# Kernel tuning notes

Hardware: AMD Instinct MI355X
Metric: run time of the kernel (lower is better)

Reference implementation:

```python
import jax, jax.numpy as jnp
import numpy as np

D_MODEL = 768
BOTTLENECK = 64
LN_EPS = 1e-5
SCALE = 1.0


def setup_inputs() -> dict:
    key = jax.random.key(0)
    k_x, k_wd = jax.random.split(key, 2)
    x = jax.random.normal(k_x, (8, 4096, D_MODEL), dtype=jnp.float32)
    # LayerNorm params (torch default init: weight=1, bias=0)
    ln_w = jnp.ones((D_MODEL,), dtype=jnp.float32)
    ln_b = jnp.zeros((D_MODEL,), dtype=jnp.float32)
    # down_proj: kaiming_uniform(a=sqrt(5)) -> bound = 1/sqrt(fan_in)
    bound = 1.0 / np.sqrt(D_MODEL)
    w_down = jax.random.uniform(k_wd, (BOTTLENECK, D_MODEL), dtype=jnp.float32,
                                minval=-bound, maxval=bound)
    b_down = jnp.zeros((BOTTLENECK,), dtype=jnp.float32)
    # up_proj initialized to zeros per the module; use small random values
    # instead so the backward test is non-degenerate? No: stay faithful but
    # zeros would kill gradients through w_down; use a tiny random up matrix
    # (mathematically same op, just different param values).
    k_wu = jax.random.fold_in(key, 7)
    w_up = 0.02 * jax.random.normal(k_wu, (D_MODEL, BOTTLENECK), dtype=jnp.float32)
    b_up = jnp.zeros((D_MODEL,), dtype=jnp.float32)
    return {"x": x, "ln_w": ln_w, "ln_b": ln_b,
            "w_down": w_down, "b_down": b_down,
            "w_up": w_up, "b_up": b_up}


def reference(x, ln_w, ln_b, w_down, b_down, w_up, b_up):
    # adapter_layernorm_option == 'in': LayerNorm first
    mu = jnp.mean(x, axis=-1, keepdims=True)
    var = jnp.mean(jnp.square(x - mu), axis=-1, keepdims=True)
    xn = (x - mu) * jax.lax.rsqrt(var + LN_EPS) * ln_w + ln_b
    # down projection + ReLU (dropout p=0 in eval -> identity)
    down = jax.nn.relu(jnp.einsum('bsd,kd->bsk', xn, w_down) + b_down)
    # up projection, scale, residual add (add_residual=True, residual=x)
    up = (jnp.einsum('bsk,dk->bsd', down, w_up) + b_up) * SCALE
    return up + x
```

## Files before the change

### kernel.cpp

```cpp
#include <hip/hip_runtime.h>

#define D_MODEL 768
#define BN 64
#define LN_EPS 1e-5f

typedef __attribute__((ext_vector_type(8))) short bf16x8;
typedef __attribute__((ext_vector_type(4))) float f32x4;

static __device__ __forceinline__ unsigned short f2bf(float f) {
    unsigned int u = __float_as_uint(f);
    u = (u + 0x7FFFu + ((u >> 16) & 1u)) >> 16;
    return (unsigned short)u;
}
static __device__ __forceinline__ float bf2f(unsigned short u) {
    return __uint_as_float(((unsigned int)u) << 16);
}

__global__ void prep(const float* __restrict__ wd, const float* __restrict__ ln_w,
                     const float* __restrict__ ln_b, const float* __restrict__ b_down,
                     const float* __restrict__ wu,
                     unsigned short* __restrict__ wd2_frag, unsigned short* __restrict__ wu_frag,
                     float* __restrict__ S, float* __restrict__ bd2) {
    const int b = blockIdx.x;
    const int t = threadIdx.x;
    const int c = b;
    const int wv = c >> 4, cl = c & 15;
    float s = 0.f, sb = 0.f;
    #pragma unroll
    for (int i = 0; i < 12; ++i) {
        const int d = t + 64 * i;
        const float w0 = wd[c * D_MODEL + d];
        const float w2 = w0 * ln_w[d];
        s  += w2;
        sb += w0 * ln_b[d];
        const int ks = d >> 5, kg = (d >> 3) & 3, e = d & 7;
        wd2_frag[(((wv * 24 + ks) * 64) + kg * 16 + cl) * 8 + e] = f2bf(w2);
    }
    #pragma unroll
    for (int off = 1; off < 64; off <<= 1) {
        s  += __shfl_xor(s, off);
        sb += __shfl_xor(sb, off);
    }
    if (t == 0) { S[c] = s; bd2[c] = b_down[c] + sb; }
    #pragma unroll
    for (int i = 0; i < 12; ++i) {
        const int n = b * 12 + i;
        const float v = wu[n * BN + t];
        const int jj = n >> 4, nl = n & 15;
        const int h = t >> 5, kg = (t >> 3) & 3, e = t & 7;
        wu_frag[(((jj * 2 + h) * 64) + kg * 16 + nl) * 8 + e] = f2bf(v);
    }
}

__global__ __launch_bounds__(256, 4) void adapter_kernel(
    const float* __restrict__ x,
    const unsigned short* __restrict__ wd2_frag, const float* __restrict__ S,
    const float* __restrict__ bd2,
    const unsigned short* __restrict__ wu_frag, const float* __restrict__ b_up,
    float* __restrict__ out)
{
    __shared__ __align__(16) unsigned short sX[16 * 768];
    __shared__ __align__(16) unsigned short sDown[16][72];
    __shared__ float sMu[16], sRs[16];

    const int tid  = threadIdx.x;
    const int lane = tid & 63;
    const int w    = tid >> 6;
    const int kg   = lane >> 4;
    const int l16  = lane & 15;
    const size_t gt0 = (size_t)blockIdx.x * 16;

    {
        float4 v[12];
        const float* base0 = x + (gt0 + w * 4) * D_MODEL + lane * 4;
        #pragma unroll
        for (int p = 0; p < 4; ++p) {
            #pragma unroll
            for (int sg = 0; sg < 3; ++sg)
                v[p * 3 + sg] = *(const float4*)(base0 + p * D_MODEL + sg * 256);
        }
        #pragma unroll
        for (int p = 0; p < 4; ++p) {
            const int r = w * 4 + p;
            float sum = 0.f, sq = 0.f;
            #pragma unroll
            for (int sg = 0; sg < 3; ++sg) {
                const float4 f = v[p * 3 + sg];
                sum += (f.x + f.y) + (f.z + f.w);
                sq  += (f.x * f.x + f.y * f.y) + (f.z * f.z + f.w * f.w);
            }
            #pragma unroll
            for (int off = 1; off < 64; off <<= 1) {
                sum += __shfl_xor(sum, off);
                sq  += __shfl_xor(sq, off);
            }
            if (lane == 0) {
                const float mu = sum * (1.f / D_MODEL);
                sMu[r] = mu;
                sRs[r] = rsqrtf(sq * (1.f / D_MODEL) - mu * mu + LN_EPS);
            }
            #pragma unroll
            for (int sg = 0; sg < 3; ++sg) {
                const float4 f = v[p * 3 + sg];
                ushort4 o;
                o.x = f2bf(f.x); o.y = f2bf(f.y); o.z = f2bf(f.z); o.w = f2bf(f.w);
                const int bytecol = ((sg * 256 + lane * 4) * 2) ^ ((r & 15) << 4);
                *(ushort4*)((char*)&sX[r * 768] + bytecol) = o;
            }
        }
    }
    __syncthreads();

    {
        const int c = w * 16 + l16;
        const unsigned short* bp = wd2_frag + ((size_t)(w * 24) * 64 + lane) * 8;
        const char* sxrow = (const char*)&sX[l16 * 768];
        f32x4 acc = {0.f, 0.f, 0.f, 0.f};
        #pragma unroll
        for (int ks = 0; ks < 24; ++ks) {
            const bf16x8 a = *(const bf16x8*)(sxrow + ((ks * 64 + kg * 16) ^ (l16 << 4)));
            const bf16x8 b = *(const bf16x8*)(bp + ks * 512);
            acc = __builtin_amdgcn_mfma_f32_16x16x32_bf16(a, b, acc, 0, 0, 0);
        }
        const float Sc = S[c], bd = bd2[c];
        #pragma unroll
        for (int r = 0; r < 4; ++r) {
            const int t = kg * 4 + r;
            const float vv = sRs[t] * (acc[r] - sMu[t] * Sc) + bd;
            sDown[t][c] = f2bf(vv > 0.f ? vv : 0.f);
        }
    }
    __syncthreads();

    {
        const bf16x8 pb0 = *(const bf16x8*)&sDown[l16][kg * 8];
        const bf16x8 pb1 = *(const bf16x8*)&sDown[l16][32 + kg * 8];
        float* orow = out + (gt0 + l16) * D_MODEL;
        const char* sxrow = (const char*)&sX[l16 * 768];
        #pragma unroll 3
        for (int j = 0; j < 12; ++j) {
            const int jj = 4 * j + w;
            const unsigned short* ap = wu_frag + ((size_t)(jj * 2) * 64 + lane) * 8;
            const bf16x8 a0 = *(const bf16x8*)ap;
            const bf16x8 a1 = *(const bf16x8*)(ap + 512);
            f32x4 acc = {0.f, 0.f, 0.f, 0.f};
            acc = __builtin_amdgcn_mfma_f32_16x16x32_bf16(a0, pb0, acc, 0, 0, 0);
            acc = __builtin_amdgcn_mfma_f32_16x16x32_bf16(a1, pb1, acc, 0, 0, 0);
            const int oc = jj * 16 + kg * 4;
            const float4 bu = *(const float4*)(b_up + oc);
            const ushort4 xb = *(const ushort4*)(sxrow + ((oc * 2) ^ (l16 << 4)));
            float4 o;
            o.x = acc[0] + bu.x + bf2f(xb.x);
            o.y = acc[1] + bu.y + bf2f(xb.y);
            o.z = acc[2] + bu.z + bf2f(xb.z);
            o.w = acc[3] + bu.w + bf2f(xb.w);
            *(float4*)(orow + oc) = o;
        }
    }
}

extern "C" void kernel_launch(void* const* d_in, const int* in_sizes, int n_in,
                              void* d_out, int out_size, void* d_ws, size_t ws_size,
                              hipStream_t stream) {
    const float* x      = (const float*)d_in[0];
    const float* ln_w   = (const float*)d_in[1];
    const float* ln_b   = (const float*)d_in[2];
    const float* w_down = (const float*)d_in[3];
    const float* b_down = (const float*)d_in[4];
    const float* w_up   = (const float*)d_in[5];
    const float* b_up   = (const float*)d_in[6];
    float* out = (float*)d_out;

    unsigned short* wd2_frag = (unsigned short*)d_ws;
    unsigned short* wu_frag  = wd2_frag + BN * D_MODEL;
    float* S   = (float*)((char*)d_ws + 2 * BN * D_MODEL * sizeof(unsigned short));
    float* bd2 = S + BN;

    prep<<<BN, 64, 0, stream>>>(w_down, ln_w, ln_b, b_down, w_up, wd2_frag, wu_frag, S, bd2);

    const int tokens = in_sizes[0] / D_MODEL;
    const int grid = tokens / 16;
    adapter_kernel<<<grid, 256, 0, stream>>>(x, wd2_frag, S, bd2, wu_frag, b_up, out);
}
```

Before: 50.51 us.

## Process two token tiles per block, prefetching the second tile during GEMMs

Each block now handles two 16-token tiles, so the grid is halved. The second tile's global loads are issued right after the first down-projection, overlapping memory latency with the epilogue and up-projection. b_up is staged in LDS, and syncs use lightweight lgkmcnt barriers. This keeps 48 extra float4 registers live across the first tile's compute, which raises register pressure and may reduce occupancy or cause spills. Fewer blocks also means less parallelism for latency hiding.

New measurement: 86.94 us. +72.1%, slower.

```diff
diff --git a/kernel.cpp b/kernel.cpp
--- a/kernel.cpp
+++ b/kernel.cpp
@@ -3,6 +3,7 @@
 #define D_MODEL 768
 #define BN 64
 #define LN_EPS 1e-5f
+#define MFMA __builtin_amdgcn_mfma_f32_16x16x32_bf16
 
 typedef __attribute__((ext_vector_type(8))) short bf16x8;
 typedef __attribute__((ext_vector_type(4))) float f32x4;
@@ -14,6 +15,12 @@
 }
 static __device__ __forceinline__ float bf2f(unsigned short u) {
     return __uint_as_float(((unsigned int)u) << 16);
+}
+
+static __device__ __forceinline__ void barrier_lds() {
+    asm volatile("s_waitcnt lgkmcnt(0)" ::: "memory");
+    __builtin_amdgcn_s_barrier();
+    asm volatile("" ::: "memory");
 }
 
 __global__ void prep(const float* __restrict__ wd, const float* __restrict__ ln_w,
@@ -52,6 +59,108 @@
     }
 }
 
+static __device__ __forceinline__ void load12(const float* __restrict__ x, size_t gt0,
+                                              int w, int lane, float4 (&v)[12]) {
+    const float* base0 = x + (gt0 + (size_t)(w * 4)) * D_MODEL + lane * 4;
+    #pragma unroll
+    for (int p = 0; p < 4; ++p)
+        #pragma unroll
+        for (int sg = 0; sg < 3; ++sg)
+            v[p * 3 + sg] = *(const float4*)(base0 + p * D_MODEL + sg * 256);
+}
+
+static __device__ __forceinline__ void stage_tile(const float4 (&v)[12], int w, int lane,
+                                                  unsigned short* sX, float* sMu, float* sRs) {
+    #pragma unroll
+    for (int p = 0; p < 4; ++p) {
+        const int r = w * 4 + p;
+        float sum = 0.f, sq = 0.f;
+        #pragma unroll
+        for (int sg = 0; sg < 3; ++sg) {
+            const float4 f = v[p * 3 + sg];
+            sum += (f.x + f.y) + (f.z + f.w);
+            sq  += (f.x * f.x + f.y * f.y) + (f.z * f.z + f.w * f.w);
+        }
+        #pragma unroll
+        for (int off = 1; off < 64; off <<= 1) {
+            sum += __shfl_xor(sum, off);
+            sq  += __shfl_xor(sq, off);
+        }
+        if (lane == 0) {
+            const float mu = sum * (1.f / D_MODEL);
+            sMu[r] = mu;
+            sRs[r] = rsqrtf(sq * (1.f / D_MODEL) - mu * mu + LN_EPS);
+        }
+        #pragma unroll
+        for (int sg = 0; sg < 3; ++sg) {
+            const float4 f = v[p * 3 + sg];
+            ushort4 o;
+            o.x = f2bf(f.x); o.y = f2bf(f.y); o.z = f2bf(f.z); o.w = f2bf(f.w);
+            const int bytecol = ((sg * 256 + lane * 4) * 2) ^ ((r & 15) << 4);
+            *(ushort4*)((char*)(sX + r * 768) + bytecol) = o;
+        }
+    }
+}
+
+static __device__ __forceinline__ f32x4 gemm1_mac(int w, int lane, int kg, int l16,
+                                                  const unsigned short* __restrict__ wd2_frag,
+                                                  const unsigned short* sX) {
+    const unsigned short* bp = wd2_frag + ((size_t)(w * 24) * 64 + lane) * 8;
+    const char* sxrow = (const char*)(sX + l16 * 768);
+    f32x4 acc = {0.f, 0.f, 0.f, 0.f};
+    #pragma unroll
+    for (int ks = 0; ks < 24; ++ks) {
+        const bf16x8 a = *(const bf16x8*)(sxrow + ((ks * 64 + kg * 16) ^ (l16 << 4)));
+        const bf16x8 b = *(const bf16x8*)(bp + ks * 512);
+        acc = MFMA(a, b, acc, 0, 0, 0);
+    }
+    return acc;
+}
+
+static __device__ __forceinline__ void gemm1_epi(f32x4 acc, int w, int kg, int l16,
+                                                 float Sc, float bd,
+                                                 const float* sMu, const float* sRs,
+                                                 unsigned short (*sDown)[72]) {
+    const int c = w * 16 + l16;
+    #pragma unroll
+    for (int r = 0; r < 4; ++r) {
+        const int t = kg * 4 + r;
+        const float vv = sRs[t] * (acc[r] - sMu[t] * Sc) + bd;
+        sDown[t][c] = f2bf(vv > 0.f ? vv : 0.f);
+    }
+}
+
+static __device__ __forceinline__ void gemm2_store(int w, int kg, int l16, size_t gt0,
+                                                   const unsigned short* __restrict__ wu_frag,
+                                                   const unsigned short* sX,
+                                                   const unsigned short (*sDown)[72],
+                                                   const float* sBup, int lane,
+                                                   float* __restrict__ out) {
+    const bf16x8 pb0 = *(const bf16x8*)&sDown[l16][kg * 8];
+    const bf16x8 pb1 = *(const bf16x8*)&sDown[l16][32 + kg * 8];
+    float* orow = out + (gt0 + l16) * D_MODEL;
+    const char* sxrow = (const char*)(sX + l16 * 768);
+    #pragma unroll 4
+    for (int j = 0; j < 12; ++j) {
+        const int jj = 4 * j + w;
+        const unsigned short* ap = wu_frag + ((size_t)(jj * 2) * 64 + lane) * 8;
+        const bf16x8 a0 = *(const bf16x8*)ap;
+        const bf16x8 a1 = *(const bf16x8*)(ap + 512);
+        f32x4 acc = {0.f, 0.f, 0.f, 0.f};
+        acc = MFMA(a0, pb0, acc, 0, 0, 0);
+        acc = MFMA(a1, pb1, acc, 0, 0, 0);
+        const int oc = jj * 16 + kg * 4;
+        const float4 bu = *(const float4*)(sBup + oc);
+        const ushort4 xb = *(const ushort4*)(sxrow + ((oc * 2) ^ (l16 << 4)));
+        float4 o;
+        o.x = acc[0] + bu.x + bf2f(xb.x);
+        o.y = acc[1] + bu.y + bf2f(xb.y);
+        o.z = acc[2] + bu.z + bf2f(xb.z);
+        o.w = acc[3] + bu.w + bf2f(xb.w);
+        *(float4*)(orow + oc) = o;
+    }
+}
+
 __global__ __launch_bounds__(256, 4) void adapter_kernel(
     const float* __restrict__ x,
     const unsigned short* __restrict__ wd2_frag, const float* __restrict__ S,
@@ -62,101 +171,44 @@
     __shared__ __align__(16) unsigned short sX[16 * 768];
     __shared__ __align__(16) unsigned short sDown[16][72];
     __shared__ float sMu[16], sRs[16];
+    __shared__ __align__(16) float sBup[D_MODEL];
 
     const int tid  = threadIdx.x;
     const int lane = tid & 63;
     const int w    = tid >> 6;
     const int kg   = lane >> 4;
     const int l16  = lane & 15;
-    const size_t gt0 = (size_t)blockIdx.x * 16;
-
-    {
-        float4 v[12];
-        const float* base0 = x + (gt0 + w * 4) * D_MODEL + lane * 4;
-        #pragma unroll
-        for (int p = 0; p < 4; ++p) {
-            #pragma unroll
-            for (int sg = 0; sg < 3; ++sg)
-                v[p * 3 + sg] = *(const float4*)(base0 + p * D_MODEL + sg * 256);
-        }
-        #pragma unroll
-        for (int p = 0; p < 4; ++p) {
-            const int r = w * 4 + p;
-            float sum = 0.f, sq = 0.f;
-            #pragma unroll
-            for (int sg = 0; sg < 3; ++sg) {
-                const float4 f = v[p * 3 + sg];
-                sum += (f.x + f.y) + (f.z + f.w);
-                sq  += (f.x * f.x + f.y * f.y) + (f.z * f.z + f.w * f.w);
-            }
-            #pragma unroll
-            for (int off = 1; off < 64; off <<= 1) {
-                sum += __shfl_xor(sum, off);
-                sq  += __shfl_xor(sq, off);
-            }
-            if (lane == 0) {
-                const float mu = sum * (1.f / D_MODEL);
-                sMu[r] = mu;
-                sRs[r] = rsqrtf(sq * (1.f / D_MODEL) - mu * mu + LN_EPS);
-            }
-            #pragma unroll
-            for (int sg = 0; sg < 3; ++sg) {
-                const float4 f = v[p * 3 + sg];
-                ushort4 o;
-                o.x = f2bf(f.x); o.y = f2bf(f.y); o.z = f2bf(f.z); o.w = f2bf(f.w);
-                const int bytecol = ((sg * 256 + lane * 4) * 2) ^ ((r & 15) << 4);
-                *(ushort4*)((char*)&sX[r * 768] + bytecol) = o;
-            }
-        }
-    }
-    __syncthreads();
-
-    {
-        const int c = w * 16 + l16;
-        const unsigned short* bp = wd2_frag + ((size_t)(w * 24) * 64 + lane) * 8;
-        const char* sxrow = (const char*)&sX[l16 * 768];
-        f32x4 acc = {0.f, 0.f, 0.f, 0.f};
-        #pragma unroll
-        for (int ks = 0; ks < 24; ++ks) {
-            const bf16x8 a = *(const bf16x8*)(sxrow + ((ks * 64 + kg * 16) ^ (l16 << 4)));
-            const bf16x8 b = *(const bf16x8*)(bp + ks * 512);
-            acc = __builtin_amdgcn_mfma_f32_16x16x32_bf16(a, b, acc, 0, 0, 0);
-        }
-        const float Sc = S[c], bd = bd2[c];
-        #pragma unroll
-        for (int r = 0; r < 4; ++r) {
-            const int t = kg * 4 + r;
-            const float vv = sRs[t] * (acc[r] - sMu[t] * Sc) + bd;
-            sDown[t][c] = f2bf(vv > 0.f ? vv : 0.f);
-        }
-    }
-    __syncthreads();
-
-    {
-        const bf16x8 pb0 = *(const bf16x8*)&sDown[l16][kg * 8];
-        const bf16x8 pb1 = *(const bf16x8*)&sDown[l16][32 + kg * 8];
-        float* orow = out + (gt0 + l16) * D_MODEL;
-        const char* sxrow = (const char*)&sX[l16 * 768];
-        #pragma unroll 3
-        for (int j = 0; j < 12; ++j) {
-            const int jj = 4 * j + w;
-            const unsigned short* ap = wu_frag + ((size_t)(jj * 2) * 64 + lane) * 8;
-            const bf16x8 a0 = *(const bf16x8*)ap;
-            const bf16x8 a1 = *(const bf16x8*)(ap + 512);
-            f32x4 acc = {0.f, 0.f, 0.f, 0.f};
-            acc = __builtin_amdgcn_mfma_f32_16x16x32_bf16(a0, pb0, acc, 0, 0, 0);
-            acc = __builtin_amdgcn_mfma_f32_16x16x32_bf16(a1, pb1, acc, 0, 0, 0);
-            const int oc = jj * 16 + kg * 4;
-            const float4 bu = *(const float4*)(b_up + oc);
-            const ushort4 xb = *(const ushort4*)(sxrow + ((oc * 2) ^ (l16 << 4)));
-            float4 o;
-            o.x = acc[0] + bu.x + bf2f(xb.x);
-            o.y = acc[1] + bu.y + bf2f(xb.y);
-            o.z = acc[2] + bu.z + bf2f(xb.z);
-            o.w = acc[3] + bu.w + bf2f(xb.w);
-            *(float4*)(orow + oc) = o;
-        }
-    }
+    const size_t gtA = (size_t)blockIdx.x * 16;
+    const size_t gtB = gtA + (size_t)gridDim.x * 16;
+
+    const int c = w * 16 + l16;
+    const float Sc = S[c], bd = bd2[c];
+    sBup[tid]       = b_up[tid];
+    sBup[tid + 256] = b_up[tid + 256];
+    sBup[tid + 512] = b_up[tid + 512];
+
+    float4 vA[12];
+    load12(x, gtA, w, lane, vA);
+    stage_tile(vA, w, lane, sX, sMu, sRs);
+    barrier_lds();
+
+    f32x4 acc1 = gemm1_mac(w, lane, kg, l16, wd2_frag, sX);
+    __builtin_amdgcn_sched_barrier(0);
+    float4 vB[12];
+    load12(x, gtB, w, lane, vB);
+    __builtin_amdgcn_sched_barrier(0);
+    gemm1_epi(acc1, w, kg, l16, Sc, bd, sMu, sRs, sDown);
+    barrier_lds();
+
+    gemm2_store(w, kg, l16, gtA, wu_frag, sX, sDown, sBup, lane, out);
+    barrier_lds();
+
+    stage_tile(vB, w, lane, sX, sMu, sRs);
+    barrier_lds();
+    f32x4 acc2 = gemm1_mac(w, lane, kg, l16, wd2_frag, sX);
+    gemm1_epi(acc2, w, kg, l16, Sc, bd, sMu, sRs, sDown);
+    barrier_lds();
+    gemm2_store(w, kg, l16, gtB, wu_frag, sX, sDown, sBup, lane, out);
 }
 
 extern "C" void kernel_launch(void* const* d_in, const int* in_sizes, int n_in,
@@ -179,6 +231,6 @@
     prep<<<BN, 64, 0, stream>>>(w_down, ln_w, ln_b, b_down, w_up, wd2_frag, wu_frag, S, bd2);
 
     const int tokens = in_sizes[0] / D_MODEL;
-    const int grid = tokens / 16;
+    const int grid = tokens / 32;
     adapter_kernel<<<grid, 256, 0, stream>>>(x, wd2_frag, S, bd2, wu_frag, b_up, out);
 }
```

## Process 32 tokens per 512-thread block and prefetch weights early

Applied to the files above, without the earlier changes.

Doubles the tile to 32 tokens per block with 8 waves, two row tiles by four column quarters, so each block's weight fragments serve more tokens. The first up-projection fragments and the per-column LN constants are loaded before the LayerNorm phase so their latency overlaps with the x loads. LDS per block roughly doubles (about 54KB), and launch bounds become 512 threads with 6 blocks, which may limit occupancy in exchange for fewer blocks and less redundant weight traffic.

Result: slower. 66.15 us (+31.0%).

```diff
diff --git a/kernel.cpp b/kernel.cpp
--- a/kernel.cpp
+++ b/kernel.cpp
@@ -3,6 +3,7 @@
 #define D_MODEL 768
 #define BN 64
 #define LN_EPS 1e-5f
+#define MFMA __builtin_amdgcn_mfma_f32_16x16x32_bf16
 
 typedef __attribute__((ext_vector_type(8))) short bf16x8;
 typedef __attribute__((ext_vector_type(4))) float f32x4;
@@ -52,80 +53,85 @@
     }
 }
 
-__global__ __launch_bounds__(256, 4) void adapter_kernel(
+__global__ __launch_bounds__(512, 6) void adapter_kernel(
     const float* __restrict__ x,
     const unsigned short* __restrict__ wd2_frag, const float* __restrict__ S,
     const float* __restrict__ bd2,
     const unsigned short* __restrict__ wu_frag, const float* __restrict__ b_up,
     float* __restrict__ out)
 {
-    __shared__ __align__(16) unsigned short sX[16 * 768];
-    __shared__ __align__(16) unsigned short sDown[16][72];
-    __shared__ float sMu[16], sRs[16];
+    __shared__ __align__(16) unsigned short sX[32 * 768];
+    __shared__ __align__(16) unsigned short sDown[32][72];
+    __shared__ float sMu[32], sRs[32];
 
     const int tid  = threadIdx.x;
     const int lane = tid & 63;
     const int w    = tid >> 6;
     const int kg   = lane >> 4;
     const int l16  = lane & 15;
-    const size_t gt0 = (size_t)blockIdx.x * 16;
+    const int cq   = w & 3;
+    const int rt   = w >> 2;
+    const size_t gt0 = (size_t)blockIdx.x * 32;
 
+    float4 v[12];
     {
-        float4 v[12];
-        const float* base0 = x + (gt0 + w * 4) * D_MODEL + lane * 4;
+        const float* base0 = x + (gt0 + (size_t)(w * 4)) * D_MODEL + lane * 4;
         #pragma unroll
-        for (int p = 0; p < 4; ++p) {
+        for (int p = 0; p < 4; ++p)
             #pragma unroll
             for (int sg = 0; sg < 3; ++sg)
                 v[p * 3 + sg] = *(const float4*)(base0 + p * D_MODEL + sg * 256);
+    }
+    const unsigned short* ap0 = wu_frag + ((size_t)(cq * 2) * 64 + lane) * 8;
+    const bf16x8 a0p = *(const bf16x8*)ap0;
+    const bf16x8 a1p = *(const bf16x8*)(ap0 + 512);
+    const int c = cq * 16 + l16;
+    const float Sc = S[c], bd = bd2[c];
+
+    #pragma unroll
+    for (int p = 0; p < 4; ++p) {
+        const int r = w * 4 + p;
+        float sum = 0.f, sq = 0.f;
+        #pragma unroll
+        for (int sg = 0; sg < 3; ++sg) {
+            const float4 f = v[p * 3 + sg];
+            sum += (f.x + f.y) + (f.z + f.w);
+            sq  += (f.x * f.x + f.y * f.y) + (f.z * f.z + f.w * f.w);
         }
         #pragma unroll
-        for (int p = 0; p < 4; ++p) {
-            const int r = w * 4 + p;
-            float sum = 0.f, sq = 0.f;
-            #pragma unroll
-            for (int sg = 0; sg < 3; ++sg) {
-                const float4 f = v[p * 3 + sg];
-                sum += (f.x + f.y) + (f.z + f.w);
-                sq  += (f.x * f.x + f.y * f.y) + (f.z * f.z + f.w * f.w);
-            }
-            #pragma unroll
-            for (int off = 1; off < 64; off <<= 1) {
-                sum += __shfl_xor(sum, off);
-                sq  += __shfl_xor(sq, off);
-            }
-            if (lane == 0) {
-                const float mu = sum * (1.f / D_MODEL);
-                sMu[r] = mu;
-                sRs[r] = rsqrtf(sq * (1.f / D_MODEL) - mu * mu + LN_EPS);
-            }
-            #pragma unroll
-            for (int sg = 0; sg < 3; ++sg) {
-                const float4 f = v[p * 3 + sg];
-                ushort4 o;
-                o.x = f2bf(f.x); o.y = f2bf(f.y); o.z = f2bf(f.z); o.w = f2bf(f.w);
-                const int bytecol = ((sg * 256 + lane * 4) * 2) ^ ((r & 15) << 4);
-                *(ushort4*)((char*)&sX[r * 768] + bytecol) = o;
-            }
+        for (int off = 1; off < 64; off <<= 1) {
+            sum += __shfl_xor(sum, off);
+            sq  += __shfl_xor(sq, off);
+        }
+        if (lane == 0) {
+            const float mu = sum * (1.f / D_MODEL);
+            sMu[r] = mu;
+            sRs[r] = rsqrtf(sq * (1.f / D_MODEL) - mu * mu + LN_EPS);
+        }
+        #pragma unroll
+        for (int sg = 0; sg < 3; ++sg) {
+            const float4 f = v[p * 3 + sg];
+            ushort4 o;
+            o.x = f2bf(f.x); o.y = f2bf(f.y); o.z = f2bf(f.z); o.w = f2bf(f.w);
+            const int bytecol = ((sg * 256 + lane * 4) * 2) ^ ((r & 15) << 4);
+            *(ushort4*)((char*)(sX + r * 768) + bytecol) = o;
         }
     }
     __syncthreads();
 
     {
-        const int c = w * 16 + l16;
-        const unsigned short* bp = wd2_frag + ((size_t)(w * 24) * 64 + lane) * 8;
-        const char* sxrow = (const char*)&sX[l16 * 768];
+        const unsigned short* bp = wd2_frag + ((size_t)(cq * 24) * 64 + lane) * 8;
+        const char* sxrow = (const char*)(sX + (rt * 16 + l16) * 768);
         f32x4 acc = {0.f, 0.f, 0.f, 0.f};
         #pragma unroll
         for (int ks = 0; ks < 24; ++ks) {
             const bf16x8 a = *(const bf16x8*)(sxrow + ((ks * 64 + kg * 16) ^ (l16 << 4)));
             const bf16x8 b = *(const bf16x8*)(bp + ks * 512);
-            acc = __builtin_amdgcn_mfma_f32_16x16x32_bf16(a, b, acc, 0, 0, 0);
+            acc = MFMA(a, b, acc, 0, 0, 0);
         }
-        const float Sc = S[c], bd = bd2[c];
         #pragma unroll
         for (int r = 0; r < 4; ++r) {
-            const int t = kg * 4 + r;
+            const int t = rt * 16 + kg * 4 + r;
             const float vv = sRs[t] * (acc[r] - sMu[t] * Sc) + bd;
             sDown[t][c] = f2bf(vv > 0.f ? vv : 0.f);
         }
@@ -133,19 +139,23 @@
     __syncthreads();
 
     {
-        const bf16x8 pb0 = *(const bf16x8*)&sDown[l16][kg * 8];
-        const bf16x8 pb1 = *(const bf16x8*)&sDown[l16][32 + kg * 8];
-        float* orow = out + (gt0 + l16) * D_MODEL;
-        const char* sxrow = (const char*)&sX[l16 * 768];
-        #pragma unroll 3
+        const bf16x8 pb0 = *(const bf16x8*)&sDown[rt * 16 + l16][kg * 8];
+        const bf16x8 pb1 = *(const bf16x8*)&sDown[rt * 16 + l16][32 + kg * 8];
+        float* orow = out + (gt0 + rt * 16 + l16) * D_MODEL;
+        const char* sxrow = (const char*)(sX + (rt * 16 + l16) * 768);
+        #pragma unroll 4
         for (int j = 0; j < 12; ++j) {
-            const int jj = 4 * j + w;
-            const unsigned short* ap = wu_frag + ((size_t)(jj * 2) * 64 + lane) * 8;
-            const bf16x8 a0 = *(const bf16x8*)ap;
-            const bf16x8 a1 = *(const bf16x8*)(ap + 512);
+            const int jj = 4 * j + cq;
+            bf16x8 a0, a1;
+            if (j == 0) { a0 = a0p; a1 = a1p; }
+            else {
+                const unsigned short* ap = wu_frag + ((size_t)(jj * 2) * 64 + lane) * 8;
+                a0 = *(const bf16x8*)ap;
+                a1 = *(const bf16x8*)(ap + 512);
+            }
             f32x4 acc = {0.f, 0.f, 0.f, 0.f};
-            acc = __builtin_amdgcn_mfma_f32_16x16x32_bf16(a0, pb0, acc, 0, 0, 0);
-            acc = __builtin_amdgcn_mfma_f32_16x16x32_bf16(a1, pb1, acc, 0, 0, 0);
+            acc = MFMA(a0, pb0, acc, 0, 0, 0);
+            acc = MFMA(a1, pb1, acc, 0, 0, 0);
             const int oc = jj * 16 + kg * 4;
             const float4 bu = *(const float4*)(b_up + oc);
             const ushort4 xb = *(const ushort4*)(sxrow + ((oc * 2) ^ (l16 << 4)));
@@ -179,6 +189,6 @@
     prep<<<BN, 64, 0, stream>>>(w_down, ln_w, ln_b, b_down, w_up, wd2_frag, wu_frag, S, bd2);
 
     const int tokens = in_sizes[0] / D_MODEL;
-    const int grid = tokens / 16;
-    adapter_kernel<<<grid, 256, 0, stream>>>(x, wd2_frag, S, bd2, wu_frag, b_up, out);
+    const int grid = tokens / 32;
+    adapter_kernel<<<grid, 512, 0, stream>>>(x, wd2_frag, S, bd2, wu_frag, b_up, out);
 }
```

## Stage up-projection in LDS and add the fp32 residual with coalesced row stores

Applied to the files above, without the earlier changes.

The up-projection result plus bias is written to shared memory as bf16 in a padded buffer. A new final phase then rereads x from global memory in fp32 and writes each output row with fully coalesced float4 stores. This replaces the old residual, which used the bf16 copy of x and produced strided per-fragment stores. The launch-bounds occupancy hint is also raised from 4 to 6 blocks. The cost is a second global read of x, which is expected to hit in cache, plus an extra barrier and bf16 rounding of the adapter output.

Result: slower. 68.12 us (+34.9%).

```diff
diff --git a/kernel.cpp b/kernel.cpp
--- a/kernel.cpp
+++ b/kernel.cpp
@@ -3,6 +3,7 @@
 #define D_MODEL 768
 #define BN 64
 #define LN_EPS 1e-5f
+#define MFMA __builtin_amdgcn_mfma_f32_16x16x32_bf16
 
 typedef __attribute__((ext_vector_type(8))) short bf16x8;
 typedef __attribute__((ext_vector_type(4))) float f32x4;
@@ -52,14 +53,14 @@
     }
 }
 
-__global__ __launch_bounds__(256, 4) void adapter_kernel(
+__global__ __launch_bounds__(256, 6) void adapter_kernel(
     const float* __restrict__ x,
     const unsigned short* __restrict__ wd2_frag, const float* __restrict__ S,
     const float* __restrict__ bd2,
     const unsigned short* __restrict__ wu_frag, const float* __restrict__ b_up,
     float* __restrict__ out)
 {
-    __shared__ __align__(16) unsigned short sX[16 * 768];
+    __shared__ __align__(16) unsigned short sBuf[16 * 776];
     __shared__ __align__(16) unsigned short sDown[16][72];
     __shared__ float sMu[16], sRs[16];
 
@@ -72,13 +73,12 @@
 
     {
         float4 v[12];
-        const float* base0 = x + (gt0 + w * 4) * D_MODEL + lane * 4;
-        #pragma unroll
-        for (int p = 0; p < 4; ++p) {
+        const float* base0 = x + (gt0 + (size_t)(w * 4)) * D_MODEL + lane * 4;
+        #pragma unroll
+        for (int p = 0; p < 4; ++p)
             #pragma unroll
             for (int sg = 0; sg < 3; ++sg)
                 v[p * 3 + sg] = *(const float4*)(base0 + p * D_MODEL + sg * 256);
-        }
         #pragma unroll
         for (int p = 0; p < 4; ++p) {
             const int r = w * 4 + p;
@@ -105,7 +105,7 @@
                 ushort4 o;
                 o.x = f2bf(f.x); o.y = f2bf(f.y); o.z = f2bf(f.z); o.w = f2bf(f.w);
                 const int bytecol = ((sg * 256 + lane * 4) * 2) ^ ((r & 15) << 4);
-                *(ushort4*)((char*)&sX[r * 768] + bytecol) = o;
+                *(ushort4*)((char*)sBuf + r * 1536 + bytecol) = o;
             }
         }
     }
@@ -114,13 +114,13 @@
     {
         const int c = w * 16 + l16;
         const unsigned short* bp = wd2_frag + ((size_t)(w * 24) * 64 + lane) * 8;
-        const char* sxrow = (const char*)&sX[l16 * 768];
+        const char* sxrow = (const char*)sBuf + l16 * 1536;
         f32x4 acc = {0.f, 0.f, 0.f, 0.f};
         #pragma unroll
         for (int ks = 0; ks < 24; ++ks) {
             const bf16x8 a = *(const bf16x8*)(sxrow + ((ks * 64 + kg * 16) ^ (l16 << 4)));
             const bf16x8 b = *(const bf16x8*)(bp + ks * 512);
-            acc = __builtin_amdgcn_mfma_f32_16x16x32_bf16(a, b, acc, 0, 0, 0);
+            acc = MFMA(a, b, acc, 0, 0, 0);
         }
         const float Sc = S[c], bd = bd2[c];
         #pragma unroll
@@ -135,26 +135,44 @@
     {
         const bf16x8 pb0 = *(const bf16x8*)&sDown[l16][kg * 8];
         const bf16x8 pb1 = *(const bf16x8*)&sDown[l16][32 + kg * 8];
-        float* orow = out + (gt0 + l16) * D_MODEL;
-        const char* sxrow = (const char*)&sX[l16 * 768];
-        #pragma unroll 3
+        #pragma unroll 4
         for (int j = 0; j < 12; ++j) {
             const int jj = 4 * j + w;
             const unsigned short* ap = wu_frag + ((size_t)(jj * 2) * 64 + lane) * 8;
             const bf16x8 a0 = *(const bf16x8*)ap;
             const bf16x8 a1 = *(const bf16x8*)(ap + 512);
             f32x4 acc = {0.f, 0.f, 0.f, 0.f};
-            acc = __builtin_amdgcn_mfma_f32_16x16x32_bf16(a0, pb0, acc, 0, 0, 0);
-            acc = __builtin_amdgcn_mfma_f32_16x16x32_bf16(a1, pb1, acc, 0, 0, 0);
+            acc = MFMA(a0, pb0, acc, 0, 0, 0);
+            acc = MFMA(a1, pb1, acc, 0, 0, 0);
             const int oc = jj * 16 + kg * 4;
             const float4 bu = *(const float4*)(b_up + oc);
-            const ushort4 xb = *(const ushort4*)(sxrow + ((oc * 2) ^ (l16 << 4)));
-            float4 o;
-            o.x = acc[0] + bu.x + bf2f(xb.x);
-            o.y = acc[1] + bu.y + bf2f(xb.y);
-            o.z = acc[2] + bu.z + bf2f(xb.z);
-            o.w = acc[3] + bu.w + bf2f(xb.w);
-            *(float4*)(orow + oc) = o;
+            ushort4 o;
+            o.x = f2bf(acc[0] + bu.x);
+            o.y = f2bf(acc[1] + bu.y);
+            o.z = f2bf(acc[2] + bu.z);
+            o.w = f2bf(acc[3] + bu.w);
+            *(ushort4*)((char*)sBuf + l16 * 1552 + oc * 2) = o;
+        }
+    }
+    __syncthreads();
+
+    {
+        const float* xrow0 = x + (gt0 + (size_t)(w * 4)) * D_MODEL + lane * 4;
+        float* orow0 = out + (gt0 + (size_t)(w * 4)) * D_MODEL + lane * 4;
+        #pragma unroll
+        for (int p = 0; p < 4; ++p) {
+            const int r = w * 4 + p;
+            #pragma unroll
+            for (int sg = 0; sg < 3; ++sg) {
+                const float4 xv = *(const float4*)(xrow0 + p * D_MODEL + sg * 256);
+                const ushort4 ub = *(const ushort4*)((char*)sBuf + r * 1552 + (sg * 256 + lane * 4) * 2);
+                float4 o;
+                o.x = xv.x + bf2f(ub.x);
+                o.y = xv.y + bf2f(ub.y);
+                o.z = xv.z + bf2f(ub.z);
+                o.w = xv.w + bf2f(ub.w);
+                *(float4*)(orow0 + p * D_MODEL + sg * 256) = o;
+            }
         }
     }
 }
```
